# Optimization experiments

Measured on AMD Instinct MI355X. Metric: run time of the kernel, lower is better.

Reference implementation:

```python
import jax, jax.numpy as jnp
import numpy as np

K_SIZE = 5


def _extract_patches(x, k):
    """im2col over a k x k neighborhood with SAME zero padding.
    x: [B, H, W, C] -> [B, H, W, k*k, C], kernel positions row-major (di, dj).
    """
    B, H, W, C = x.shape
    pad = k // 2
    xp = jnp.pad(x, ((0, 0), (pad, pad), (pad, pad), (0, 0)))
    shifts = [xp[:, i:i + H, j:j + W, :] for i in range(k) for j in range(k)]
    return jnp.stack(shifts, axis=3)  # [B, H, W, k*k, C]


def setup_inputs() -> dict:
    key = jax.random.key(0)
    k1, k2, k3 = jax.random.split(key, 3)
    B, H, W, BINS = 4, 128, 128, 64
    attn = jax.random.uniform(k1, (B, H, W, K_SIZE * K_SIZE + 1), dtype=jnp.float32)
    ref_value = jax.random.normal(k2, (B, H, W, BINS), dtype=jnp.float32)
    current_ref_value = jax.random.normal(k3, (B, H, W, BINS), dtype=jnp.float32)
    return {"attn": attn, "ref_value": ref_value, "current_ref_value": current_ref_value}


def reference(attn, ref_value, current_ref_value):
    # [B, H, W, k*k, bins]: neighbor values gathered im2col-style
    ref_stacked = _extract_patches(ref_value, K_SIZE)
    # append the current value as the (k*k+1)-th aggregation slot
    ref_stacked = jnp.concatenate(
        [ref_stacked, current_ref_value[:, :, :, None, :]], axis=-2
    )  # [B, H, W, k*k+1, bins]
    # weighted sum over the k*k+1 neighbor slots
    return jnp.einsum('bhwk,bhwki->bhwi', attn, ref_stacked)
```

## Files before the change

### kernel.cpp

```cpp
#include <hip/hip_runtime.h>


#define KS     5
#define NSLOT  26
#define BINS   64
#define PIX_PER_BLOCK 16

__global__ __launch_bounds__(256) void agg_kernel(
    const float* __restrict__ attn,
    const float* __restrict__ ref,
    const float* __restrict__ cur,
    float* __restrict__ out,
    int B, int H, int W)
{
    __shared__ float s_attn[PIX_PER_BLOCK * NSLOT];

    const int tid = threadIdx.x;
    const int block_pix0 = blockIdx.x * PIX_PER_BLOCK;

    if (tid < (PIX_PER_BLOCK * NSLOT / 4)) {
        ((float4*)s_attn)[tid] =
            ((const float4*)(attn + (size_t)block_pix0 * NSLOT))[tid];
    }
    __syncthreads();

    const int pix_local = tid >> 4;
    const int q         = tid & 15;
    const int pix = block_pix0 + pix_local;

    const int w  = pix % W;
    const int hw = pix / W;
    const int h  = hw % H;
    const int b  = hw / H;

    const float* wv = s_attn + pix_local * NSLOT;
    const int binoff = q * 4;

    float4 acc = make_float4(0.f, 0.f, 0.f, 0.f);

    const size_t row_base = ((size_t)b * H) * W;

#pragma unroll
    for (int di = 0; di < KS; ++di) {
        const int hh  = h + di - 2;
        const bool hok = (hh >= 0) && (hh < H);
        const int hc  = min(max(hh, 0), H - 1);
        const size_t hrow = (row_base + (size_t)hc * W);
#pragma unroll
        for (int dj = 0; dj < KS; ++dj) {
            const int ww  = w + dj - 2;
            const bool ok = hok && (ww >= 0) && (ww < W);
            const int wc  = min(max(ww, 0), W - 1);
            const float wgt = ok ? wv[di * KS + dj] : 0.0f;
            const float4 v = *(const float4*)(ref + (hrow + wc) * BINS + binoff);
            acc.x += wgt * v.x;
            acc.y += wgt * v.y;
            acc.z += wgt * v.z;
            acc.w += wgt * v.w;
        }
    }

    {
        const float wgt = wv[KS * KS];
        const float4 v = *(const float4*)(cur + (size_t)pix * BINS + binoff);
        acc.x += wgt * v.x;
        acc.y += wgt * v.y;
        acc.z += wgt * v.z;
        acc.w += wgt * v.w;
    }

    *(float4*)(out + (size_t)pix * BINS + binoff) = acc;
}

extern "C" void kernel_launch(void* const* d_in, const int* in_sizes, int n_in,
                              void* d_out, int out_size, void* d_ws, size_t ws_size,
                              hipStream_t stream) {
    const float* attn = (const float*)d_in[0];
    const float* ref  = (const float*)d_in[1];
    const float* cur  = (const float*)d_in[2];
    float* out = (float*)d_out;

    const int B = 4, H = 128, W = 128;
    const int pixels = B * H * W;
    const int blocks = pixels / PIX_PER_BLOCK;

    agg_kernel<<<blocks, 256, 0, stream>>>(attn, ref, cur, out, B, H, W);
}
```

Before: 92.26 us.

## Tile 4x16 pixel blocks to reuse neighbor row loads across output rows

Each block now covers a 4-row by 16-column tile, and each thread computes four output rows for one column and bin quad. Each input row is loaded once per thread as five horizontal neighbors and reused across up to four output rows, which cuts redundant global loads of ref. Attention weights are rearranged in shared memory with out-of-range columns pre-zeroed, so inner-loop masking goes away. The cost is more registers, fewer blocks (1024), and a scalar, uncoalesced attn staging loop.

```diff
diff --git a/kernel.cpp b/kernel.cpp
--- a/kernel.cpp
+++ b/kernel.cpp
@@ -1,75 +1,105 @@
 #include <hip/hip_runtime.h>
 
 
-#define KS     5
-#define NSLOT  26
-#define BINS   64
-#define PIX_PER_BLOCK 16
+#define KS    5
+#define NSLOT 26
+#define BINS  64
+#define TW    16
+#define TH    4
 
 __global__ __launch_bounds__(256) void agg_kernel(
     const float* __restrict__ attn,
     const float* __restrict__ ref,
     const float* __restrict__ cur,
-    float* __restrict__ out,
-    int B, int H, int W)
+    float* __restrict__ out)
 {
-    __shared__ float s_attn[PIX_PER_BLOCK * NSLOT];
+    constexpr int H = 128, W = 128;
+
+    __shared__ __align__(16) float s_w[TH * KS * TW * 8];
+    __shared__ float s_w25[TH * TW];
 
     const int tid = threadIdx.x;
-    const int block_pix0 = blockIdx.x * PIX_PER_BLOCK;
+    const int blk = blockIdx.x;
+    const int w0 = (blk & 7) * TW;
+    const int h0 = ((blk >> 3) & 31) * TH;
+    const int b  = blk >> 8;
 
-    if (tid < (PIX_PER_BLOCK * NSLOT / 4)) {
-        ((float4*)s_attn)[tid] =
-            ((const float4*)(attn + (size_t)block_pix0 * NSLOT))[tid];
+    const size_t pix00 = ((size_t)b * H + h0) * W + w0;
+
+    for (int i = tid; i < TH * TW * NSLOT; i += 256) {
+        const int rl   = i / (TW * NSLOT);
+        const int rem  = i - rl * (TW * NSLOT);
+        const int wl   = rem / NSLOT;
+        const int slot = rem - wl * NSLOT;
+        float v = attn[(pix00 + (size_t)rl * W + wl) * NSLOT + slot];
+        if (slot == NSLOT - 1) {
+            s_w25[rl * TW + wl] = v;
+        } else {
+            const int di = slot / KS;
+            const int dj = slot - di * KS;
+            const int ww = w0 + wl - 2 + dj;
+            if (ww < 0 || ww >= W) v = 0.0f;
+            s_w[((rl * KS + di) * TW + wl) * 8 + dj] = v;
+        }
     }
     __syncthreads();
 
-    const int pix_local = tid >> 4;
-    const int q         = tid & 15;
-    const int pix = block_pix0 + pix_local;
+    const int wg = tid >> 4;
+    const int q  = tid & 15;
+    const int binoff = q * 4;
+    const int w = w0 + wg;
 
-    const int w  = pix % W;
-    const int hw = pix / W;
-    const int h  = hw % H;
-    const int b  = hw / H;
+    int wcoff[KS];
+#pragma unroll
+    for (int dj = 0; dj < KS; ++dj) {
+        int ww = w - 2 + dj;
+        ww = min(max(ww, 0), W - 1);
+        wcoff[dj] = ww * BINS + binoff;
+    }
 
-    const float* wv = s_attn + pix_local * NSLOT;
-    const int binoff = q * 4;
+    float4 acc[TH];
+#pragma unroll
+    for (int rl = 0; rl < TH; ++rl) acc[rl] = make_float4(0.f, 0.f, 0.f, 0.f);
 
-    float4 acc = make_float4(0.f, 0.f, 0.f, 0.f);
-
-    const size_t row_base = ((size_t)b * H) * W;
+    const size_t brow = (size_t)b * H * W;
 
 #pragma unroll
-    for (int di = 0; di < KS; ++di) {
-        const int hh  = h + di - 2;
-        const bool hok = (hh >= 0) && (hh < H);
-        const int hc  = min(max(hh, 0), H - 1);
-        const size_t hrow = (row_base + (size_t)hc * W);
+    for (int hi = 0; hi < TH + 4; ++hi) {
+        const int hh = h0 - 2 + hi;
+        if (hh < 0 || hh >= H) continue;
+        const float* rowp = ref + (brow + (size_t)hh * W) * BINS;
+
+        float4 v[KS];
 #pragma unroll
-        for (int dj = 0; dj < KS; ++dj) {
-            const int ww  = w + dj - 2;
-            const bool ok = hok && (ww >= 0) && (ww < W);
-            const int wc  = min(max(ww, 0), W - 1);
-            const float wgt = ok ? wv[di * KS + dj] : 0.0f;
-            const float4 v = *(const float4*)(ref + (hrow + wc) * BINS + binoff);
-            acc.x += wgt * v.x;
-            acc.y += wgt * v.y;
-            acc.z += wgt * v.z;
-            acc.w += wgt * v.w;
+        for (int dj = 0; dj < KS; ++dj)
+            v[dj] = *(const float4*)(rowp + wcoff[dj]);
+
+#pragma unroll
+        for (int rl = 0; rl < TH; ++rl) {
+            const int di = hi - rl;
+            if (di < 0 || di > 4) continue;
+            const float* wp = &s_w[((rl * KS + di) * TW + wg) * 8];
+            const float4 w03 = *(const float4*)wp;
+            const float  w4  = wp[4];
+            acc[rl].x += w03.x * v[0].x + w03.y * v[1].x + w03.z * v[2].x + w03.w * v[3].x + w4 * v[4].x;
+            acc[rl].y += w03.x * v[0].y + w03.y * v[1].y + w03.z * v[2].y + w03.w * v[3].y + w4 * v[4].y;
+            acc[rl].z += w03.x * v[0].z + w03.y * v[1].z + w03.z * v[2].z + w03.w * v[3].z + w4 * v[4].z;
+            acc[rl].w += w03.x * v[0].w + w03.y * v[1].w + w03.z * v[2].w + w03.w * v[3].w + w4 * v[4].w;
         }
     }
 
-    {
-        const float wgt = wv[KS * KS];
-        const float4 v = *(const float4*)(cur + (size_t)pix * BINS + binoff);
-        acc.x += wgt * v.x;
-        acc.y += wgt * v.y;
-        acc.z += wgt * v.z;
-        acc.w += wgt * v.w;
+#pragma unroll
+    for (int rl = 0; rl < TH; ++rl) {
+        const float wgt = s_w25[rl * TW + wg];
+        const size_t p = pix00 + (size_t)rl * W + wg;
+        const float4 v = *(const float4*)(cur + p * BINS + binoff);
+        float4 a = acc[rl];
+        a.x += wgt * v.x;
+        a.y += wgt * v.y;
+        a.z += wgt * v.z;
+        a.w += wgt * v.w;
+        *(float4*)(out + p * BINS + binoff) = a;
     }
-
-    *(float4*)(out + (size_t)pix * BINS + binoff) = acc;
 }
 
 extern "C" void kernel_launch(void* const* d_in, const int* in_sizes, int n_in,
@@ -80,9 +110,5 @@
     const float* cur  = (const float*)d_in[2];
     float* out = (float*)d_out;
 
-    const int B = 4, H = 128, W = 128;
-    const int pixels = B * H * W;
-    const int blocks = pixels / PIX_PER_BLOCK;
-
-    agg_kernel<<<blocks, 256, 0, stream>>>(attn, ref, cur, out, B, H, W);
+    agg_kernel<<<1024, 256, 0, stream>>>(attn, ref, cur, out);
 }
```

After: 91.48 us. About the same (-0.8%).
